# Kernel optimization log

Hardware: AMD Instinct MI355X
Metric: run time of the kernel (lower is better)

## Reference

```python
import jax, jax.numpy as jnp
import numpy as np

D = 256
H = 8

def setup_inputs() -> dict:
    key = jax.random.key(0)
    ks = jax.random.split(key, 6)
    b, n = 4, 2048
    X = jax.random.normal(ks[0], (b, n, D), dtype=jnp.float32)
    s = 1.0 / np.sqrt(D)
    Wq = jax.random.normal(ks[1], (D, D * H), dtype=jnp.float32) * s
    Wk = jax.random.normal(ks[2], (D, D * H), dtype=jnp.float32) * s
    Wv = jax.random.normal(ks[3], (D, D * H), dtype=jnp.float32) * s
    Wo = jax.random.normal(ks[4], (D * H, D), dtype=jnp.float32) * (1.0 / np.sqrt(D * H))
    bo = jnp.zeros((D,), dtype=jnp.float32)
    return {"X": X, "Wq": Wq, "Wk": Wk, "Wv": Wv, "Wo": Wo, "bo": bo}

def reference(X, Wq, Wk, Wv, Wo, bo):
    b, n, _ = X.shape
    scale = D ** (-0.25)
    # project and split heads: [b, n, H, D]
    q = (X @ Wq).reshape(b, n, H, D) * scale
    k = (X @ Wk).reshape(b, n, H, D) * scale
    v = (X @ Wv).reshape(b, n, H, D)
    # attention scores [b, H, n, n]
    scores = jnp.einsum("bqhd,bkhd->bhqk", q, k)
    attn = jax.nn.softmax(scores, axis=-1)
    out = jnp.einsum("bhqk,bkhd->bqhd", attn, v).reshape(b, n, H * D)
    return out @ Wo + bo
```

## Files before the change

### kernel.cpp

```cpp
#include <hip/hip_runtime.h>
#include <hip/hip_bf16.h>
#include <stdint.h>


using short8 = __attribute__((ext_vector_type(8))) short;
using f32x4  = __attribute__((ext_vector_type(4))) float;
using f32x16 = __attribute__((ext_vector_type(16))) float;

#define MFMA16(a, b, c) __builtin_amdgcn_mfma_f32_16x16x32_bf16((a), (b), (c), 0, 0, 0)
#define MFMA32(a, b, c) __builtin_amdgcn_mfma_f32_32x32x16_bf16((a), (b), (c), 0, 0, 0)

#if __has_builtin(__builtin_amdgcn_exp2f)
#define EXP2(x) __builtin_amdgcn_exp2f(x)
#else
#define EXP2(x) exp2f(x)
#endif

__device__ __forceinline__ uint16_t f2bf(float f) {
  union { float f; uint32_t u; } v; v.f = f;
  uint32_t u = v.u;
  u += 0x7fffu + ((u >> 16) & 1u);
  return (uint16_t)(u >> 16);
}

__device__ __forceinline__ uint32_t cvtpk_bf16(float lo, float hi) {
  uint32_t r;
  asm("v_cvt_pk_bf16_f32 %0, %1, %2" : "=v"(r) : "v"(lo), "v"(hi));
  return r;
}

__device__ __forceinline__ void swap32(uint32_t& a, uint32_t& b) {
  asm volatile("v_permlane32_swap_b32 %0, %1" : "+v"(a), "+v"(b));
}

__device__ __forceinline__ void gll16(const void* g, void* l) {
  __builtin_amdgcn_global_load_lds(
      (const __attribute__((address_space(1))) void*)g,
      (__attribute__((address_space(3))) void*)l, 16, 0, 0);
}

__global__ __launch_bounds__(256) void cast_x_k(const float* __restrict__ X,
                                                uint16_t* __restrict__ Xb, int n4) {
  int i = blockIdx.x * 256 + threadIdx.x;
  if (i >= n4) return;
  float4 v = ((const float4*)X)[i];
  union { uint16_t u[4]; uint2 p; } r;
  r.u[0] = f2bf(v.x); r.u[1] = f2bf(v.y); r.u[2] = f2bf(v.z); r.u[3] = f2bf(v.w);
  ((uint2*)Xb)[i] = r.p;
}

__global__ __launch_bounds__(256) void tcast_k(const float* __restrict__ W,
                                               uint16_t* __restrict__ Wt,
                                               int R, int C, float scale) {
  __shared__ float T[64][65];
  int c0 = blockIdx.x * 64, r0 = blockIdx.y * 64;
  int tid = threadIdx.x;
  int cc = tid & 63;
  for (int rr = tid >> 6; rr < 64; rr += 4)
    T[rr][cc] = W[(size_t)(r0 + rr) * C + c0 + cc];
  __syncthreads();
  int n = tid >> 2, kb = (tid & 3) * 16;
  uint16_t* orow = Wt + (size_t)(c0 + n) * R + r0 + kb;
#pragma unroll
  for (int j = 0; j < 16; ++j) orow[j] = f2bf(T[kb + j][n] * scale);
}

template <int EPI>
__global__ __launch_bounds__(256) void gemm_bt_k(const uint16_t* __restrict__ A,
                                                 const uint16_t* __restrict__ Bt,
                                                 void* __restrict__ Cv,
                                                 const float* __restrict__ bias,
                                                 int M, int N, int K) {
  __shared__ uint16_t As[128 * 64];
  __shared__ uint16_t Bs[128 * 64];
  const int tid = threadIdx.x;
  const int wv = tid >> 6, lane = tid & 63;
  const int ql = lane & 15, gq = lane >> 4;
  const int wr = wv >> 1, wc = wv & 1;
  const int m0 = blockIdx.y * 128, n0 = blockIdx.x * 128;

  f32x4 acc[4][4];
#pragma unroll
  for (int i = 0; i < 4; ++i)
#pragma unroll
    for (int j = 0; j < 4; ++j) acc[i][j] = (f32x4){0.f, 0.f, 0.f, 0.f};

  const int nkb = K >> 6;
  for (int kb = 0; kb < nkb; ++kb) {
#pragma unroll
    for (int j = 0; j < 4; ++j) {
      int s = (wv * 4 + j) * 64 + lane;
      int row = s >> 3, c = s & 7;
      int gc = c ^ (row & 7);
      gll16(A + (size_t)(m0 + row) * K + kb * 64 + gc * 8, &As[(wv * 4 + j) * 512]);
      gll16(Bt + (size_t)(n0 + row) * K + kb * 64 + gc * 8, &Bs[(wv * 4 + j) * 512]);
    }
    __syncthreads();

    short8 af[4][2], bf[4][2];
#pragma unroll
    for (int mt = 0; mt < 4; ++mt)
#pragma unroll
      for (int kk = 0; kk < 2; ++kk) {
        int row = wr * 64 + mt * 16 + ql;
        int c = (kk * 4 + gq) ^ (row & 7);
        af[mt][kk] = *(const short8*)&As[row * 64 + c * 8];
      }
#pragma unroll
    for (int nt = 0; nt < 4; ++nt)
#pragma unroll
      for (int kk = 0; kk < 2; ++kk) {
        int row = wc * 64 + nt * 16 + ql;
        int c = (kk * 4 + gq) ^ (row & 7);
        bf[nt][kk] = *(const short8*)&Bs[row * 64 + c * 8];
      }
#pragma unroll
    for (int kk = 0; kk < 2; ++kk)
#pragma unroll
      for (int mt = 0; mt < 4; ++mt)
#pragma unroll
        for (int nt = 0; nt < 4; ++nt)
          acc[mt][nt] = MFMA16(af[mt][kk], bf[nt][kk], acc[mt][nt]);
    __syncthreads();
  }

#pragma unroll
  for (int mt = 0; mt < 4; ++mt)
#pragma unroll
    for (int nt = 0; nt < 4; ++nt)
#pragma unroll
      for (int r = 0; r < 4; ++r) {
        int m = m0 + wr * 64 + mt * 16 + gq * 4 + r;
        int n = n0 + wc * 64 + nt * 16 + ql;
        float v = acc[mt][nt][r];
        if (EPI == 0) {
          ((uint16_t*)Cv)[(size_t)m * N + n] = f2bf(v);
        } else {
          ((float*)Cv)[(size_t)m * N + n] = v + bias[n];
        }
      }
}

__global__ __launch_bounds__(512, 2) void attn2_k(const uint16_t* __restrict__ qk,
                                                  const uint16_t* __restrict__ vtws,
                                                  uint16_t* __restrict__ ctx,
                                                  int b0, int nb) {
  __shared__ uint16_t Ks[2][64 * 256];
  __shared__ uint16_t Vts[2][256 * 64];
  const int S = 2048;
  const int h = blockIdx.x & 7;
  const int t = blockIdx.x >> 3;
  const int bb = t >> 3, qb = t & 7;
  const int tid = threadIdx.x, w = tid >> 6, lane = tid & 63;
  const int l31 = lane & 31, hi = lane >> 5;
  const size_t SN = (size_t)nb * S;

  short8 qf[16];
  {
    const uint16_t* qrow =
        qk + (size_t)(bb * S + qb * 256 + w * 32 + l31) * 4096 + h * 256 + hi * 8;
#pragma unroll
    for (int ds = 0; ds < 16; ++ds) qf[ds] = *(const short8*)(qrow + ds * 16);
  }

  uint32_t ok[4], ov[4];
#pragma unroll
  for (int j = 0; j < 4; ++j) {
    int s = (j * 8 + w) * 64 + lane;
    int krw = s >> 5, kc = s & 31;
    int kgc = kc ^ (krw & 7);
    ok[j] = (uint32_t)(((bb * S + krw) * 4096 + 2048 + h * 256 + kgc * 8) * 2);
    int d = s >> 3, vc = s & 7;
    int vgc = vc ^ (d & 7);
    ov[j] = (uint32_t)((((h * 256 + d) * SN) + (size_t)bb * S + vgc * 8) * 2);
  }
  const uint32_t kstep = 64 * 4096 * 2;
  const uint32_t vstep = 64 * 2;

  const char* kgbase = (const char*)qk;
  const char* vgbase = (const char*)vtws;

  auto stageK = [&](int buf, int kb) {
#pragma unroll
    for (int j = 0; j < 4; ++j)
      gll16(kgbase + ok[j] + (uint32_t)kb * kstep, &Ks[buf][(j * 8 + w) * 512]);
  };
  auto stageV = [&](int buf, int kb) {
#pragma unroll
    for (int j = 0; j < 4; ++j)
      gll16(vgbase + ov[j] + (uint32_t)kb * vstep, &Vts[buf][(j * 8 + w) * 512]);
  };

  f32x16 cacc[8];
#pragma unroll
  for (int db = 0; db < 8; ++db)
#pragma unroll
    for (int r = 0; r < 16; ++r) cacc[db][r] = 0.f;
  float m_run = -3e38f, l_run = 0.f;
  short8 pa0, pa1, pa2, pa3;

  const int rx = (l31 & 7) << 4;
  const int hi16 = hi << 4;

  f32x16 sA, sB;

  auto qk_only = [&](int cur) {
    const char* kr0 = (const char*)Ks[cur] + l31 * 512;
    const char* kr1 = kr0 + 32 * 512;
#pragma unroll
    for (int r = 0; r < 16; ++r) { sA[r] = 0.f; sB[r] = 0.f; }
    __builtin_amdgcn_s_setprio(1);
#pragma unroll
    for (int i = 0; i < 16; ++i) {
      int off = (i * 32 + hi16) ^ rx;
      sA = MFMA32(*(const short8*)(kr0 + off), qf[i], sA);
      sB = MFMA32(*(const short8*)(kr1 + off), qf[i], sB);
    }
    __builtin_amdgcn_s_setprio(0);
  };

  auto qk_pv = [&](int cur) {
    const char* kr0 = (const char*)Ks[cur] + l31 * 512;
    const char* kr1 = kr0 + 32 * 512;
    const char* vb = (const char*)Vts[cur ^ 1];
#pragma unroll
    for (int r = 0; r < 16; ++r) { sA[r] = 0.f; sB[r] = 0.f; }
    __builtin_amdgcn_s_setprio(1);
#pragma unroll
    for (int i = 0; i < 16; ++i) {
      int off = (i * 32 + hi16) ^ rx;
      sA = MFMA32(*(const short8*)(kr0 + off), qf[i], sA);
      sB = MFMA32(*(const short8*)(kr1 + off), qf[i], sB);
#pragma unroll
      for (int u = 0; u < 2; ++u) {
        const int idx = 2 * i + u;
        const int ks = idx >> 3, db = idx & 7;
        int voff = (ks * 32 + hi16) ^ rx;
        short8 vf = *(const short8*)(vb + (db * 32 + l31) * 128 + voff);
        short8 p = (ks == 0) ? pa0 : (ks == 1) ? pa1 : (ks == 2) ? pa2 : pa3;
        cacc[db] = MFMA32(p, vf, cacc[db]);
      }
    }
    __builtin_amdgcn_s_setprio(0);
  };

  auto pv_only = [&](int slot) {
    const char* vb = (const char*)Vts[slot];
    __builtin_amdgcn_s_setprio(1);
#pragma unroll
    for (int ks = 0; ks < 4; ++ks) {
      int voff = (ks * 32 + hi16) ^ rx;
      short8 p = (ks == 0) ? pa0 : (ks == 1) ? pa1 : (ks == 2) ? pa2 : pa3;
#pragma unroll
      for (int db = 0; db < 8; ++db) {
        short8 vf = *(const short8*)(vb + (db * 32 + l31) * 128 + voff);
        cacc[db] = MFMA32(p, vf, cacc[db]);
      }
    }
    __builtin_amdgcn_s_setprio(0);
  };

  auto sm_pack = [&]() {
    float pm = fmaxf(
        fmaxf(fmaxf(fmaxf(sA[0], sA[1]), fmaxf(sA[2], sA[3])),
              fmaxf(fmaxf(sA[4], sA[5]), fmaxf(sA[6], sA[7]))),
        fmaxf(fmaxf(fmaxf(sA[8], sA[9]), fmaxf(sA[10], sA[11])),
              fmaxf(fmaxf(sA[12], sA[13]), fmaxf(sA[14], sA[15]))));
    float pmB = fmaxf(
        fmaxf(fmaxf(fmaxf(sB[0], sB[1]), fmaxf(sB[2], sB[3])),
              fmaxf(fmaxf(sB[4], sB[5]), fmaxf(sB[6], sB[7]))),
        fmaxf(fmaxf(fmaxf(sB[8], sB[9]), fmaxf(sB[10], sB[11])),
              fmaxf(fmaxf(sB[12], sB[13]), fmaxf(sB[14], sB[15]))));
    pm = fmaxf(pm, pmB);
    pm = fmaxf(pm, __shfl_xor(pm, 32));

    if (__any(pm - m_run > 8.0f)) {
      float mn = fmaxf(m_run, pm);
      float al = EXP2(m_run - mn);
      m_run = mn;
      l_run *= al;
#pragma unroll
      for (int r = 0; r < 16; ++r) {
        float a = __shfl(al, (r & 3) + 8 * (r >> 2) + 4 * hi);
#pragma unroll
        for (int db = 0; db < 8; ++db) cacc[db][r] *= a;
      }
    }

    float ps = 0.f;
#pragma unroll
    for (int r = 0; r < 16; ++r) { sA[r] = EXP2(sA[r] - m_run); ps += sA[r]; }
#pragma unroll
    for (int r = 0; r < 16; ++r) { sB[r] = EXP2(sB[r] - m_run); ps += sB[r]; }
    ps += __shfl_xor(ps, 32);
    l_run += ps;

    uint32_t WA[4][2], WB[4][2];
#pragma unroll
    for (int g = 0; g < 4; ++g) {
      WA[g][0] = cvtpk_bf16(sA[4 * g], sA[4 * g + 1]);
      WA[g][1] = cvtpk_bf16(sA[4 * g + 2], sA[4 * g + 3]);
      WB[g][0] = cvtpk_bf16(sB[4 * g], sB[4 * g + 1]);
      WB[g][1] = cvtpk_bf16(sB[4 * g + 2], sB[4 * g + 3]);
    }
    swap32(WA[0][0], WA[1][0]); swap32(WA[0][1], WA[1][1]);
    swap32(WA[2][0], WA[3][0]); swap32(WA[2][1], WA[3][1]);
    swap32(WB[0][0], WB[1][0]); swap32(WB[0][1], WB[1][1]);
    swap32(WB[2][0], WB[3][0]); swap32(WB[2][1], WB[3][1]);
    union U { uint32_t u[4]; short8 v; };
    U a0, a1, b0, b1;
    a0.u[0] = WA[0][0]; a0.u[1] = WA[0][1]; a0.u[2] = WA[1][0]; a0.u[3] = WA[1][1];
    a1.u[0] = WA[2][0]; a1.u[1] = WA[2][1]; a1.u[2] = WA[3][0]; a1.u[3] = WA[3][1];
    b0.u[0] = WB[0][0]; b0.u[1] = WB[0][1]; b0.u[2] = WB[1][0]; b0.u[3] = WB[1][1];
    b1.u[0] = WB[2][0]; b1.u[1] = WB[2][1]; b1.u[2] = WB[3][0]; b1.u[3] = WB[3][1];
    pa0 = a0.v; pa1 = a1.v; pa2 = b0.v; pa3 = b1.v;
  };

  stageK(0, 0);
  __syncthreads();

  stageK(1, 1);
  stageV(0, 0);
  qk_only(0);
  sm_pack();
  __syncthreads();

  for (int tt = 1; tt < 32; ++tt) {
    const int cur = tt & 1;
    if (tt < 31) stageK(cur ^ 1, tt + 1);
    stageV(cur, tt);
    qk_pv(cur);
    sm_pack();
    __syncthreads();
  }
  pv_only(1);

  float linv = 1.f / l_run;
  uint16_t* crow = ctx + (size_t)((b0 + bb) * S + qb * 256 + w * 32) * 2048 + h * 256;
#pragma unroll
  for (int r = 0; r < 16; ++r) {
    int qr = (r & 3) + 8 * (r >> 2) + 4 * hi;
    float lr = __shfl(linv, qr);
#pragma unroll
    for (int db = 0; db < 8; ++db)
      crow[(size_t)qr * 2048 + db * 32 + l31] = f2bf(cacc[db][r] * lr);
  }
}

extern "C" void kernel_launch(void* const* d_in, const int* in_sizes, int n_in,
                              void* d_out, int out_size, void* d_ws, size_t ws_size,
                              hipStream_t stream) {
  const float* X  = (const float*)d_in[0];
  const float* Wq = (const float*)d_in[1];
  const float* Wk = (const float*)d_in[2];
  const float* Wv = (const float*)d_in[3];
  const float* Wo = (const float*)d_in[4];
  const float* bo = (const float*)d_in[5];
  float* out = (float*)d_out;

  const int B = 4, S = 2048, Dm = 256, DH = 2048;
  (void)in_sizes; (void)n_in; (void)out_size; (void)ws_size;

  uint16_t* p = (uint16_t*)d_ws;
  uint16_t* Xb  = p; p += (size_t)B * S * Dm;
  uint16_t* Wqt = p; p += (size_t)DH * Dm;
  uint16_t* Wkt = p; p += (size_t)DH * Dm;
  uint16_t* Wvt = p; p += (size_t)DH * Dm;
  uint16_t* Wot = p; p += (size_t)Dm * DH;
  uint16_t* ctx = p; p += (size_t)B * S * DH;
  uint16_t* qkw = p; p += (size_t)B * S * (2 * DH);
  uint16_t* vtws = p;

  const float qs = 0.25f * 1.2011224087864498f;

  cast_x_k<<<dim3((B * S * Dm / 4 + 255) / 256), 256, 0, stream>>>(X, Xb, B * S * Dm / 4);
  tcast_k<<<dim3(DH / 64, Dm / 64), 256, 0, stream>>>(Wq, Wqt, Dm, DH, qs);
  tcast_k<<<dim3(DH / 64, Dm / 64), 256, 0, stream>>>(Wk, Wkt, Dm, DH, qs);
  tcast_k<<<dim3(DH / 64, Dm / 64), 256, 0, stream>>>(Wv, Wvt, Dm, DH, 1.0f);
  tcast_k<<<dim3(Dm / 64, DH / 64), 256, 0, stream>>>(Wo, Wot, DH, Dm, 1.0f);

  gemm_bt_k<0><<<dim3((2 * DH) / 128, (B * S) / 128), 256, 0, stream>>>(
      Xb, Wqt, qkw, nullptr, B * S, 2 * DH, Dm);
  gemm_bt_k<0><<<dim3((B * S) / 128, DH / 128), 256, 0, stream>>>(
      Wvt, Xb, vtws, nullptr, DH, B * S, Dm);
  attn2_k<<<dim3(64 * B), 512, 0, stream>>>(qkw, vtws, ctx, 0, B);
  gemm_bt_k<1><<<dim3(Dm / 128, (B * S) / 128), 256, 0, stream>>>(
      ctx, Wot, out, bo, B * S, Dm, DH);
}
```

Measured before the change: 270.7 us.

## Shrink attention tiles to 128 queries and 32 keys per block

Retiles the flash-attention kernel so each block has 4 waves and covers 128 query rows, streaming K/V in 32-key chunks instead of 64. The grid doubles to 512 blocks and shared memory per block is reduced, which gives more blocks to spread across the 256 CUs and more resident blocks per CU. In exchange K/V tiles are reloaded by twice as many blocks, there are twice as many loop iterations and barriers, and each QK step issues half as many MFMAs between softmax steps. The LDS swizzles are rewritten to match the new 32-wide tiles.

```diff
diff --git a/kernel.cpp b/kernel.cpp
--- a/kernel.cpp
+++ b/kernel.cpp
@@ -141,16 +141,16 @@
       }
 }
 
-__global__ __launch_bounds__(512, 2) void attn2_k(const uint16_t* __restrict__ qk,
+__global__ __launch_bounds__(256, 2) void attn2_k(const uint16_t* __restrict__ qk,
                                                   const uint16_t* __restrict__ vtws,
                                                   uint16_t* __restrict__ ctx,
                                                   int b0, int nb) {
-  __shared__ uint16_t Ks[2][64 * 256];
-  __shared__ uint16_t Vts[2][256 * 64];
+  __shared__ uint16_t Ks[2][32 * 256];
+  __shared__ uint16_t Vts[2][256 * 32];
   const int S = 2048;
   const int h = blockIdx.x & 7;
   const int t = blockIdx.x >> 3;
-  const int bb = t >> 3, qb = t & 7;
+  const int bb = t >> 4, qb = t & 15;
   const int tid = threadIdx.x, w = tid >> 6, lane = tid & 63;
   const int l31 = lane & 31, hi = lane >> 5;
   const size_t SN = (size_t)nb * S;
@@ -158,7 +158,7 @@
   short8 qf[16];
   {
     const uint16_t* qrow =
-        qk + (size_t)(bb * S + qb * 256 + w * 32 + l31) * 4096 + h * 256 + hi * 8;
+        qk + (size_t)(bb * S + qb * 128 + w * 32 + l31) * 4096 + h * 256 + hi * 8;
 #pragma unroll
     for (int ds = 0; ds < 16; ++ds) qf[ds] = *(const short8*)(qrow + ds * 16);
   }
@@ -166,16 +166,16 @@
   uint32_t ok[4], ov[4];
 #pragma unroll
   for (int j = 0; j < 4; ++j) {
-    int s = (j * 8 + w) * 64 + lane;
+    int s = (j * 4 + w) * 64 + lane;
     int krw = s >> 5, kc = s & 31;
-    int kgc = kc ^ (krw & 7);
+    int kgc = kc ^ krw;
     ok[j] = (uint32_t)(((bb * S + krw) * 4096 + 2048 + h * 256 + kgc * 8) * 2);
-    int d = s >> 3, vc = s & 7;
-    int vgc = vc ^ (d & 7);
-    ov[j] = (uint32_t)((((h * 256 + d) * SN) + (size_t)bb * S + vgc * 8) * 2);
-  }
-  const uint32_t kstep = 64 * 4096 * 2;
-  const uint32_t vstep = 64 * 2;
+    int d = s >> 2, vc = s & 3;
+    int cg = vc ^ (d & 3);
+    ov[j] = (uint32_t)((((h * 256 + d) * SN) + (size_t)bb * S + cg * 8) * 2);
+  }
+  const uint32_t kstep = 32 * 4096 * 2;
+  const uint32_t vstep = 32 * 2;
 
   const char* kgbase = (const char*)qk;
   const char* vgbase = (const char*)vtws;
@@ -183,12 +183,12 @@
   auto stageK = [&](int buf, int kb) {
 #pragma unroll
     for (int j = 0; j < 4; ++j)
-      gll16(kgbase + ok[j] + (uint32_t)kb * kstep, &Ks[buf][(j * 8 + w) * 512]);
+      gll16(kgbase + ok[j] + (uint32_t)kb * kstep, &Ks[buf][(j * 4 + w) * 512]);
   };
   auto stageV = [&](int buf, int kb) {
 #pragma unroll
     for (int j = 0; j < 4; ++j)
-      gll16(vgbase + ov[j] + (uint32_t)kb * vstep, &Vts[buf][(j * 8 + w) * 512]);
+      gll16(vgbase + ov[j] + (uint32_t)kb * vstep, &Vts[buf][(j * 4 + w) * 512]);
   };
 
   f32x16 cacc[8];
@@ -197,49 +197,41 @@
 #pragma unroll
     for (int r = 0; r < 16; ++r) cacc[db][r] = 0.f;
   float m_run = -3e38f, l_run = 0.f;
-  short8 pa0, pa1, pa2, pa3;
-
-  const int rx = (l31 & 7) << 4;
+  short8 pa0, pa1;
+
+  const int kx = l31 << 4;
+  const int vx = (l31 & 3) << 4;
   const int hi16 = hi << 4;
 
-  f32x16 sA, sB;
+  f32x16 sA;
 
   auto qk_only = [&](int cur) {
-    const char* kr0 = (const char*)Ks[cur] + l31 * 512;
-    const char* kr1 = kr0 + 32 * 512;
-#pragma unroll
-    for (int r = 0; r < 16; ++r) { sA[r] = 0.f; sB[r] = 0.f; }
+    const char* kr = (const char*)Ks[cur] + l31 * 512;
+#pragma unroll
+    for (int r = 0; r < 16; ++r) sA[r] = 0.f;
     __builtin_amdgcn_s_setprio(1);
 #pragma unroll
     for (int i = 0; i < 16; ++i) {
-      int off = (i * 32 + hi16) ^ rx;
-      sA = MFMA32(*(const short8*)(kr0 + off), qf[i], sA);
-      sB = MFMA32(*(const short8*)(kr1 + off), qf[i], sB);
+      int off = (i * 32 + hi16) ^ kx;
+      sA = MFMA32(*(const short8*)(kr + off), qf[i], sA);
     }
     __builtin_amdgcn_s_setprio(0);
   };
 
   auto qk_pv = [&](int cur) {
-    const char* kr0 = (const char*)Ks[cur] + l31 * 512;
-    const char* kr1 = kr0 + 32 * 512;
+    const char* kr = (const char*)Ks[cur] + l31 * 512;
     const char* vb = (const char*)Vts[cur ^ 1];
 #pragma unroll
-    for (int r = 0; r < 16; ++r) { sA[r] = 0.f; sB[r] = 0.f; }
+    for (int r = 0; r < 16; ++r) sA[r] = 0.f;
     __builtin_amdgcn_s_setprio(1);
 #pragma unroll
     for (int i = 0; i < 16; ++i) {
-      int off = (i * 32 + hi16) ^ rx;
-      sA = MFMA32(*(const short8*)(kr0 + off), qf[i], sA);
-      sB = MFMA32(*(const short8*)(kr1 + off), qf[i], sB);
-#pragma unroll
-      for (int u = 0; u < 2; ++u) {
-        const int idx = 2 * i + u;
-        const int ks = idx >> 3, db = idx & 7;
-        int voff = (ks * 32 + hi16) ^ rx;
-        short8 vf = *(const short8*)(vb + (db * 32 + l31) * 128 + voff);
-        short8 p = (ks == 0) ? pa0 : (ks == 1) ? pa1 : (ks == 2) ? pa2 : pa3;
-        cacc[db] = MFMA32(p, vf, cacc[db]);
-      }
+      int off = (i * 32 + hi16) ^ kx;
+      sA = MFMA32(*(const short8*)(kr + off), qf[i], sA);
+      const int ks = i >> 3, db = i & 7;
+      int voff = ((ks * 2 + hi) << 4) ^ vx;
+      short8 vf = *(const short8*)(vb + (db * 32 + l31) * 64 + voff);
+      cacc[db] = MFMA32(ks ? pa1 : pa0, vf, cacc[db]);
     }
     __builtin_amdgcn_s_setprio(0);
   };
@@ -248,12 +240,12 @@
     const char* vb = (const char*)Vts[slot];
     __builtin_amdgcn_s_setprio(1);
 #pragma unroll
-    for (int ks = 0; ks < 4; ++ks) {
-      int voff = (ks * 32 + hi16) ^ rx;
-      short8 p = (ks == 0) ? pa0 : (ks == 1) ? pa1 : (ks == 2) ? pa2 : pa3;
+    for (int ks = 0; ks < 2; ++ks) {
+      int voff = ((ks * 2 + hi) << 4) ^ vx;
+      short8 p = ks ? pa1 : pa0;
 #pragma unroll
       for (int db = 0; db < 8; ++db) {
-        short8 vf = *(const short8*)(vb + (db * 32 + l31) * 128 + voff);
+        short8 vf = *(const short8*)(vb + (db * 32 + l31) * 64 + voff);
         cacc[db] = MFMA32(p, vf, cacc[db]);
       }
     }
@@ -266,12 +258,6 @@
               fmaxf(fmaxf(sA[4], sA[5]), fmaxf(sA[6], sA[7]))),
         fmaxf(fmaxf(fmaxf(sA[8], sA[9]), fmaxf(sA[10], sA[11])),
               fmaxf(fmaxf(sA[12], sA[13]), fmaxf(sA[14], sA[15]))));
-    float pmB = fmaxf(
-        fmaxf(fmaxf(fmaxf(sB[0], sB[1]), fmaxf(sB[2], sB[3])),
-              fmaxf(fmaxf(sB[4], sB[5]), fmaxf(sB[6], sB[7]))),
-        fmaxf(fmaxf(fmaxf(sB[8], sB[9]), fmaxf(sB[10], sB[11])),
-              fmaxf(fmaxf(sB[12], sB[13]), fmaxf(sB[14], sB[15]))));
-    pm = fmaxf(pm, pmB);
     pm = fmaxf(pm, __shfl_xor(pm, 32));
 
     if (__any(pm - m_run > 8.0f)) {
@@ -290,30 +276,22 @@
     float ps = 0.f;
 #pragma unroll
     for (int r = 0; r < 16; ++r) { sA[r] = EXP2(sA[r] - m_run); ps += sA[r]; }
-#pragma unroll
-    for (int r = 0; r < 16; ++r) { sB[r] = EXP2(sB[r] - m_run); ps += sB[r]; }
     ps += __shfl_xor(ps, 32);
     l_run += ps;
 
-    uint32_t WA[4][2], WB[4][2];
+    uint32_t W[4][2];
 #pragma unroll
     for (int g = 0; g < 4; ++g) {
-      WA[g][0] = cvtpk_bf16(sA[4 * g], sA[4 * g + 1]);
-      WA[g][1] = cvtpk_bf16(sA[4 * g + 2], sA[4 * g + 3]);
-      WB[g][0] = cvtpk_bf16(sB[4 * g], sB[4 * g + 1]);
-      WB[g][1] = cvtpk_bf16(sB[4 * g + 2], sB[4 * g + 3]);
-    }
-    swap32(WA[0][0], WA[1][0]); swap32(WA[0][1], WA[1][1]);
-    swap32(WA[2][0], WA[3][0]); swap32(WA[2][1], WA[3][1]);
-    swap32(WB[0][0], WB[1][0]); swap32(WB[0][1], WB[1][1]);
-    swap32(WB[2][0], WB[3][0]); swap32(WB[2][1], WB[3][1]);
+      W[g][0] = cvtpk_bf16(sA[4 * g], sA[4 * g + 1]);
+      W[g][1] = cvtpk_bf16(sA[4 * g + 2], sA[4 * g + 3]);
+    }
+    swap32(W[0][0], W[1][0]); swap32(W[0][1], W[1][1]);
+    swap32(W[2][0], W[3][0]); swap32(W[2][1], W[3][1]);
     union U { uint32_t u[4]; short8 v; };
-    U a0, a1, b0, b1;
-    a0.u[0] = WA[0][0]; a0.u[1] = WA[0][1]; a0.u[2] = WA[1][0]; a0.u[3] = WA[1][1];
-    a1.u[0] = WA[2][0]; a1.u[1] = WA[2][1]; a1.u[2] = WA[3][0]; a1.u[3] = WA[3][1];
-    b0.u[0] = WB[0][0]; b0.u[1] = WB[0][1]; b0.u[2] = WB[1][0]; b0.u[3] = WB[1][1];
-    b1.u[0] = WB[2][0]; b1.u[1] = WB[2][1]; b1.u[2] = WB[3][0]; b1.u[3] = WB[3][1];
-    pa0 = a0.v; pa1 = a1.v; pa2 = b0.v; pa3 = b1.v;
+    U a0, a1;
+    a0.u[0] = W[0][0]; a0.u[1] = W[0][1]; a0.u[2] = W[1][0]; a0.u[3] = W[1][1];
+    a1.u[0] = W[2][0]; a1.u[1] = W[2][1]; a1.u[2] = W[3][0]; a1.u[3] = W[3][1];
+    pa0 = a0.v; pa1 = a1.v;
   };
 
   stageK(0, 0);
@@ -325,9 +303,9 @@
   sm_pack();
   __syncthreads();
 
-  for (int tt = 1; tt < 32; ++tt) {
+  for (int tt = 1; tt < 64; ++tt) {
     const int cur = tt & 1;
-    if (tt < 31) stageK(cur ^ 1, tt + 1);
+    if (tt < 63) stageK(cur ^ 1, tt + 1);
     stageV(cur, tt);
     qk_pv(cur);
     sm_pack();
@@ -336,7 +314,7 @@
   pv_only(1);
 
   float linv = 1.f / l_run;
-  uint16_t* crow = ctx + (size_t)((b0 + bb) * S + qb * 256 + w * 32) * 2048 + h * 256;
+  uint16_t* crow = ctx + (size_t)((b0 + bb) * S + qb * 128 + w * 32) * 2048 + h * 256;
 #pragma unroll
   for (int r = 0; r < 16; ++r) {
     int qr = (r & 3) + 8 * (r >> 2) + 4 * hi;
@@ -383,7 +361,7 @@
       Xb, Wqt, qkw, nullptr, B * S, 2 * DH, Dm);
   gemm_bt_k<0><<<dim3((B * S) / 128, DH / 128), 256, 0, stream>>>(
       Wvt, Xb, vtws, nullptr, DH, B * S, Dm);
-  attn2_k<<<dim3(64 * B), 512, 0, stream>>>(qkw, vtws, ctx, 0, B);
+  attn2_k<<<dim3(512), 256, 0, stream>>>(qkw, vtws, ctx, 0, B);
   gemm_bt_k<1><<<dim3(Dm / 128, (B * S) / 128), 256, 0, stream>>>(
       ctx, Wot, out, bo, B * S, Dm, DH);
 }
```

Measured after the change: 265.3 us. 2.0% less time.
